# Kernel tuning notes

Measured on AMD Instinct MI355X. Metric: run time of the kernel, lower is better.

The kernel has to match this reference:

```python
import jax, jax.numpy as jnp
import numpy as np

B, T, HID = 2, 2048, 2048
H, HKV, HD = 16, 4, 128
GROUPS = H // HKV  # num_query_groups
THETA = 10000.0
SCALE = HD ** -0.5


def setup_inputs() -> dict:
    key = jax.random.key(0)
    ks = jax.random.split(key, 5)
    std = 0.02
    return {
        "x": jax.random.normal(ks[0], (B, T, HID), jnp.float32),
        "Wq": jax.random.normal(ks[1], (HID, H * HD), jnp.float32) * std,
        "Wk": jax.random.normal(ks[2], (HID, HKV * HD), jnp.float32) * std,
        "Wv": jax.random.normal(ks[3], (HID, HKV * HD), jnp.float32) * std,
        "Wo": jax.random.normal(ks[4], (H * HD, HID), jnp.float32) * std,
    }


def _rope(x):
    # x: [B, heads, T, HD]; standard LLaMA-style rotate-half RoPE
    t = x.shape[2]
    inv_freq = 1.0 / (THETA ** (jnp.arange(0, HD, 2, dtype=jnp.float32) / HD))  # [HD/2]
    ang = jnp.arange(t, dtype=jnp.float32)[:, None] * inv_freq[None, :]  # [T, HD/2]
    cos = jnp.concatenate([jnp.cos(ang), jnp.cos(ang)], axis=-1)[None, None]  # [1,1,T,HD]
    sin = jnp.concatenate([jnp.sin(ang), jnp.sin(ang)], axis=-1)[None, None]
    x1, x2 = jnp.split(x, 2, axis=-1)
    rot = jnp.concatenate([-x2, x1], axis=-1)
    return x * cos + rot * sin


def reference(x, Wq, Wk, Wv, Wo):
    b, t, _ = x.shape
    q = (x @ Wq).reshape(b, t, H, HD).transpose(0, 2, 1, 3)      # [B,H,T,HD]
    k = (x @ Wk).reshape(b, t, HKV, HD).transpose(0, 2, 1, 3)    # [B,HKV,T,HD]
    v = (x @ Wv).reshape(b, t, HKV, HD).transpose(0, 2, 1, 3)
    q = _rope(q)
    k = _rope(k)
    # GQA: repeat_interleave kv heads along head dim
    k = jnp.repeat(k, GROUPS, axis=1)  # [B,H,T,HD]
    v = jnp.repeat(v, GROUPS, axis=1)
    scores = jnp.einsum("bhqd,bhkd->bhqk", q, k) * SCALE  # [B,H,T,T]
    causal = jnp.tril(jnp.ones((t, t), dtype=bool))
    scores = jnp.where(causal[None, None], scores, jnp.finfo(scores.dtype).min)
    attn = jax.nn.softmax(scores, axis=-1)
    out = jnp.einsum("bhqk,bhkd->bhqd", attn, v)  # [B,H,T,HD]
    out = out.transpose(0, 2, 1, 3).reshape(b, t, H * HD)
    return out @ Wo
```

## Files before the change

kernel.cpp:

```cpp
#include <hip/hip_runtime.h>
#include <hip/hip_bf16.h>

#define B_   2
#define T_   2048
#define HID_ 2048
#define H_   16
#define HKV_ 4
#define HD_  128
#define NQKV 3072
#define M_   4096
#define SCALE_ 0.08838834764831845f

using f32x4 = __attribute__((ext_vector_type(4))) float;
using s16x8 = __attribute__((ext_vector_type(8))) short;
using u16x8 = __attribute__((ext_vector_type(8))) unsigned short;

typedef const __attribute__((address_space(1))) unsigned int* gptr_t;
typedef __attribute__((address_space(3))) unsigned int* lptr_t;

__device__ __forceinline__ unsigned short f2bf(float f) {
  __hip_bfloat16 h = __float2bfloat16(f);
  return *reinterpret_cast<unsigned short*>(&h);
}
__device__ __forceinline__ float bf2f(unsigned short u) {
  union { unsigned int u; float f; } x;
  x.u = ((unsigned int)u) << 16;
  return x.f;
}

__global__ void cast_bf16_k(const float* __restrict__ in, unsigned short* __restrict__ out, int n8) {
  int i = blockIdx.x * 256 + threadIdx.x;
  if (i >= n8) return;
  float4 v0 = ((const float4*)in)[i * 2];
  float4 v1 = ((const float4*)in)[i * 2 + 1];
  u16x8 o;
  o[0] = f2bf(v0.x); o[1] = f2bf(v0.y); o[2] = f2bf(v0.z); o[3] = f2bf(v0.w);
  o[4] = f2bf(v1.x); o[5] = f2bf(v1.y); o[6] = f2bf(v1.z); o[7] = f2bf(v1.w);
  ((u16x8*)out)[i] = o;
}

__global__ void transpose_cast_k(const float* __restrict__ in, unsigned short* __restrict__ out,
                                 int R, int C) {
  __shared__ float tile[32][33];
  const int tc = blockIdx.x * 32, tr = blockIdx.y * 32;
  const int lx = threadIdx.x & 31, ly = threadIdx.x >> 5;
#pragma unroll
  for (int i = 0; i < 32; i += 8) tile[ly + i][lx] = in[(long)(tr + ly + i) * C + tc + lx];
  __syncthreads();
#pragma unroll
  for (int i = 0; i < 32; i += 8)
    out[(long)(tc + ly + i) * R + tr + lx] = f2bf(tile[lx][ly + i]);
}

__global__ void transpose_v_k(const unsigned short* __restrict__ qkv, unsigned short* __restrict__ vtp) {
  __shared__ unsigned short tile[32][33];
  const int b = blockIdx.z;
  const int t0 = blockIdx.x * 32, n0 = blockIdx.y * 32;
  const int lx = threadIdx.x & 31, ly = threadIdx.x >> 5;
#pragma unroll
  for (int i = 0; i < 32; i += 8)
    tile[ly + i][lx] = qkv[(long)(b * T_ + t0 + ly + i) * NQKV + 2560 + n0 + lx];
  __syncthreads();
#pragma unroll
  for (int i = 0; i < 32; i += 8)
    vtp[(long)(b * 512 + n0 + ly + i) * T_ + t0 + lx] = tile[lx][ly + i];
}

__global__ void rope_table_k(float* __restrict__ cosT, float* __restrict__ sinT) {
  int idx = blockIdx.x * 256 + threadIdx.x;
  int tt = idx >> 6, i = idx & 63;
  float inv = powf(10000.0f, -(float)i * (1.0f / 64.0f));
  float ang = (float)tt * inv;
  cosT[idx] = cosf(ang);
  sinT[idx] = sinf(ang);
}

__global__ void rope_apply_k(unsigned short* __restrict__ qkv,
                             const float* __restrict__ cosT, const float* __restrict__ sinT) {
  int idx = blockIdx.x * 256 + threadIdx.x;
  int g = idx & 7;
  int r = idx >> 3;
  int hh = r % 20;
  int m = r / 20;
  int tt = m & (T_ - 1);
  int col = ((hh < 16) ? hh * 128 : 2048 + (hh - 16) * 128) + g * 8;
  float scl = (hh < 16) ? SCALE_ : 1.0f;
  unsigned short* p = qkv + (long)m * NQKV + col;
  u16x8 lo = *(const u16x8*)(p);
  u16x8 hi = *(const u16x8*)(p + 64);
  const float4* cp = (const float4*)(cosT + tt * 64 + g * 8);
  const float4* sp = (const float4*)(sinT + tt * 64 + g * 8);
  float c[8], s[8];
  { float4 a = cp[0], b = cp[1]; c[0]=a.x;c[1]=a.y;c[2]=a.z;c[3]=a.w;c[4]=b.x;c[5]=b.y;c[6]=b.z;c[7]=b.w; }
  { float4 a = sp[0], b = sp[1]; s[0]=a.x;s[1]=a.y;s[2]=a.z;s[3]=a.w;s[4]=b.x;s[5]=b.y;s[6]=b.z;s[7]=b.w; }
  u16x8 olo, ohi;
#pragma unroll
  for (int j = 0; j < 8; ++j) {
    float x0 = bf2f(lo[j]), x1 = bf2f(hi[j]);
    olo[j] = f2bf((x0 * c[j] - x1 * s[j]) * scl);
    ohi[j] = f2bf((x1 * c[j] + x0 * s[j]) * scl);
  }
  *(u16x8*)(p) = olo;
  *(u16x8*)(p + 64) = ohi;
}

template <bool BF16OUT>
__global__ __launch_bounds__(256) void gemm_bt(const short* __restrict__ A, const short* __restrict__ Bt,
                                               void* __restrict__ Cv, int M, int N, int K) {
  __shared__ short lA[4096];
  __shared__ short lB[4096];
  const int t = threadIdx.x;
  const int l = t & 63;
  const int w = t >> 6;
  const int wr = (w >> 1) * 64, wc = (w & 1) * 64;
  const int lr = l & 15, lk = (l >> 4) * 8;

  const short* Ag = A + (long)(blockIdx.x * 128 + (t >> 2)) * K + (t & 3) * 8;
  const short* Bg = Bt + (long)(blockIdx.y * 128 + (t >> 2)) * K + (t & 3) * 8;

  f32x4 acc[4][4] = {};

  for (int k0 = 0; k0 < K; k0 += 32) {
    __builtin_amdgcn_global_load_lds((gptr_t)(Ag + k0),                (lptr_t)&lA[t * 8],        16, 0, 0);
    __builtin_amdgcn_global_load_lds((gptr_t)(Ag + (long)64 * K + k0), (lptr_t)&lA[2048 + t * 8], 16, 0, 0);
    __builtin_amdgcn_global_load_lds((gptr_t)(Bg + k0),                (lptr_t)&lB[t * 8],        16, 0, 0);
    __builtin_amdgcn_global_load_lds((gptr_t)(Bg + (long)64 * K + k0), (lptr_t)&lB[2048 + t * 8], 16, 0, 0);
    __syncthreads();
    s16x8 af[4], bfr[4];
#pragma unroll
    for (int m = 0; m < 4; ++m) af[m] = *(const s16x8*)&lA[(wr + m * 16 + lr) * 32 + lk];
#pragma unroll
    for (int n = 0; n < 4; ++n) bfr[n] = *(const s16x8*)&lB[(wc + n * 16 + lr) * 32 + lk];
#pragma unroll
    for (int m = 0; m < 4; ++m)
#pragma unroll
      for (int n = 0; n < 4; ++n)
        acc[m][n] = __builtin_amdgcn_mfma_f32_16x16x32_bf16(af[m], bfr[n], acc[m][n], 0, 0, 0);
    __syncthreads();
  }

#pragma unroll
  for (int m = 0; m < 4; ++m) {
    const int row0 = blockIdx.x * 128 + wr + m * 16 + (l >> 4) * 4;
#pragma unroll
    for (int n = 0; n < 4; ++n) {
      const int col = blockIdx.y * 128 + wc + n * 16 + lr;
#pragma unroll
      for (int r = 0; r < 4; ++r) {
        float v = acc[m][n][r];
        if constexpr (BF16OUT)
          ((unsigned short*)Cv)[(long)(row0 + r) * N + col] = f2bf(v);
        else
          ((float*)Cv)[(long)(row0 + r) * N + col] = v;
      }
    }
  }
}

__global__ __launch_bounds__(256, 2) void attn_kernel(const short* __restrict__ qkv,
                                                      const short* __restrict__ vt,
                                                      unsigned short* __restrict__ outp) {
  const int pj = blockIdx.x;
  const int bh = blockIdx.y;
  const int b = bh >> 4, h = bh & 15, hkv = h >> 2;
  const int tid = threadIdx.x, w = tid >> 6, l = tid & 63;
  const int lr = l & 15, lg = l >> 4;

  __shared__ short lK[2][8192];
  __shared__ short lP[4][16 * 72];

  const short* kb = qkv + (long)(b * T_) * NQKV + 2048 + hkv * HD_;
  const short* vb = vt + (long)(b * 512 + hkv * HD_) * T_;
  short* pw = &lP[w][0];

  auto STAGE = [&](int buf, int kvt) {
#pragma unroll
    for (int i = 0; i < 4; ++i) {
      int flat16 = i * 256 + tid;
      int r = flat16 >> 4;
      int cb = (flat16 & 15) << 4;
      int scb = cb ^ ((r & 7) << 4);
      const short* src = kb + (long)(kvt * 64 + r) * NQKV + (scb >> 1);
      __builtin_amdgcn_global_load_lds((gptr_t)src, (lptr_t)&lK[buf][flat16 * 8], 16, 0, 0);
    }
  };

#pragma unroll 1
  for (int ph = 0; ph < 2; ++ph) {
    const int qtile = ph ? 31 - pj : pj;
    const int ntiles = qtile + 1;

    const short* qp = qkv + (long)(b * T_ + qtile * 64 + w * 16 + lr) * NQKV + h * HD_;
    s16x8 qf[4];
#pragma unroll
    for (int ks = 0; ks < 4; ++ks) qf[ks] = *(const s16x8*)(qp + ks * 32 + lg * 8);

    f32x4 o[8] = {};
    float mrun[4], lrun[4];
#pragma unroll
    for (int r = 0; r < 4; ++r) { mrun[r] = -1e30f; lrun[r] = 0.f; }

    STAGE(0, 0);
    __syncthreads();
    int cur = 0;

    for (int kvt = 0; kvt < ntiles; ++kvt) {
      if (kvt + 1 < ntiles) STAGE(cur ^ 1, kvt + 1);

      s16x8 vf[2][8];
#pragma unroll
      for (int ks2 = 0; ks2 < 2; ++ks2)
#pragma unroll
        for (int db = 0; db < 8; ++db)
          vf[ks2][db] = *(const s16x8*)(vb + (long)(db * 16 + lr) * T_ + kvt * 64 + ks2 * 32 + lg * 8);

      const char* lkb = (const char*)&lK[cur][0];
      f32x4 s[4] = {};
#pragma unroll
      for (int nb = 0; nb < 4; ++nb) {
        const int row = nb * 16 + lr;
        const int rb = row * 256;
        const int xr = (row & 7) << 4;
#pragma unroll
        for (int ks = 0; ks < 4; ++ks) {
          s16x8 kf = *(const s16x8*)(lkb + (rb + ((ks * 64 + lg * 16) ^ xr)));
          s[nb] = __builtin_amdgcn_mfma_f32_16x16x32_bf16(qf[ks], kf, s[nb], 0, 0, 0);
        }
      }
      if (kvt == qtile) {
#pragma unroll
        for (int nb = 0; nb < 4; ++nb)
#pragma unroll
          for (int r = 0; r < 4; ++r)
            if (nb * 16 + lr > w * 16 + lg * 4 + r) s[nb][r] = -1e30f;
      }
      float sc[4];
#pragma unroll
      for (int r = 0; r < 4; ++r) {
        float v = fmaxf(fmaxf(s[0][r], s[1][r]), fmaxf(s[2][r], s[3][r]));
        v = fmaxf(v, __shfl_xor(v, 1));
        v = fmaxf(v, __shfl_xor(v, 2));
        v = fmaxf(v, __shfl_xor(v, 4));
        v = fmaxf(v, __shfl_xor(v, 8));
        float mnew = fmaxf(mrun[r], v);
        sc[r] = __expf(mrun[r] - mnew);
        mrun[r] = mnew;
      }
      float ps[4] = {0.f, 0.f, 0.f, 0.f};
#pragma unroll
      for (int nb = 0; nb < 4; ++nb)
#pragma unroll
        for (int r = 0; r < 4; ++r) {
          float p = __expf(s[nb][r] - mrun[r]);
          s[nb][r] = p;
          ps[r] += p;
        }
#pragma unroll
      for (int r = 0; r < 4; ++r) {
        ps[r] += __shfl_xor(ps[r], 1);
        ps[r] += __shfl_xor(ps[r], 2);
        ps[r] += __shfl_xor(ps[r], 4);
        ps[r] += __shfl_xor(ps[r], 8);
        lrun[r] = lrun[r] * sc[r] + ps[r];
      }
#pragma unroll
      for (int db = 0; db < 8; ++db)
#pragma unroll
        for (int r = 0; r < 4; ++r) o[db][r] *= sc[r];
#pragma unroll
      for (int nb = 0; nb < 4; ++nb)
#pragma unroll
        for (int r = 0; r < 4; ++r)
          pw[(lg * 4 + r) * 72 + nb * 16 + lr] = (short)f2bf(s[nb][r]);
#pragma unroll
      for (int ks2 = 0; ks2 < 2; ++ks2) {
        s16x8 pf = *(const s16x8*)&pw[lr * 72 + ks2 * 32 + lg * 8];
#pragma unroll
        for (int db = 0; db < 8; ++db)
          o[db] = __builtin_amdgcn_mfma_f32_16x16x32_bf16(pf, vf[ks2][db], o[db], 0, 0, 0);
      }
      __syncthreads();
      cur ^= 1;
    }

    unsigned short* ob = outp + (long)(b * T_ + qtile * 64 + w * 16) * HID_ + h * HD_;
#pragma unroll
    for (int db = 0; db < 8; ++db)
#pragma unroll
      for (int r = 0; r < 4; ++r)
        ob[(long)(lg * 4 + r) * HID_ + db * 16 + lr] = f2bf(o[db][r] / lrun[r]);
  }
}

extern "C" void kernel_launch(void* const* d_in, const int* in_sizes, int n_in,
                              void* d_out, int out_size, void* d_ws, size_t ws_size,
                              hipStream_t stream) {
  (void)in_sizes; (void)n_in; (void)out_size; (void)ws_size;
  const float* x  = (const float*)d_in[0];
  const float* Wq = (const float*)d_in[1];
  const float* Wk = (const float*)d_in[2];
  const float* Wv = (const float*)d_in[3];
  const float* Wo = (const float*)d_in[4];
  float* outp = (float*)d_out;

  char* wsp = (char*)d_ws;
  auto take = [&](size_t bytes) { char* p = wsp; wsp += (bytes + 255) & ~(size_t)255; return p; };
  unsigned short* xb    = (unsigned short*)take((size_t)M_ * HID_ * 2);
  unsigned short* WqkvT = (unsigned short*)take((size_t)NQKV * HID_ * 2);
  unsigned short* WoT   = (unsigned short*)take((size_t)HID_ * HID_ * 2);
  unsigned short* QKV   = (unsigned short*)take((size_t)M_ * NQKV * 2);
  unsigned short* Vtb   = (unsigned short*)take((size_t)1024 * T_ * 2);
  unsigned short* AO    = (unsigned short*)take((size_t)M_ * HID_ * 2);
  float* cosT = (float*)take((size_t)T_ * 64 * 4);
  float* sinT = (float*)take((size_t)T_ * 64 * 4);

  cast_bf16_k<<<4096, 256, 0, stream>>>(x, xb, M_ * HID_ / 8);
  transpose_cast_k<<<dim3(64, 64), 256, 0, stream>>>(Wq, WqkvT, 2048, 2048);
  transpose_cast_k<<<dim3(16, 64), 256, 0, stream>>>(Wk, WqkvT + (size_t)2048 * 2048, 2048, 512);
  transpose_cast_k<<<dim3(16, 64), 256, 0, stream>>>(Wv, WqkvT + (size_t)2560 * 2048, 2048, 512);
  transpose_cast_k<<<dim3(64, 64), 256, 0, stream>>>(Wo, WoT, 2048, 2048);
  rope_table_k<<<512, 256, 0, stream>>>(cosT, sinT);

  gemm_bt<true><<<dim3(32, 24), 256, 0, stream>>>((const short*)xb, (const short*)WqkvT,
                                                  (void*)QKV, M_, NQKV, HID_);
  rope_apply_k<<<(M_ * 20 * 8) / 256, 256, 0, stream>>>(QKV, cosT, sinT);
  transpose_v_k<<<dim3(64, 16, 2), 256, 0, stream>>>(QKV, Vtb);

  attn_kernel<<<dim3(16, 32), 256, 0, stream>>>((const short*)QKV, (const short*)Vtb, AO);

  gemm_bt<false><<<dim3(32, 16), 256, 0, stream>>>((const short*)AO, (const short*)WoT,
                                                   (void*)outp, M_, HID_, HID_);
}
```

Baseline: 398.7 us.

## Replace GEMMs with larger-tile triple-buffered kernel and split attention query tiles

Both projection GEMMs now use a templated 512-thread kernel with 256x256 or 256x128 tiles, a three-stage LDS ring with swizzled layout, explicit vmcnt waits and MFMA priority boosting. The goal is more reuse per block and less time stalled on global loads. The attention kernel no longer pairs two query tiles per block; it launches one block per query tile, heaviest first, and raises the occupancy hint to 3. This gives finer load balancing, but some blocks become short and the large GEMM tiles leave fewer blocks to fill the CUs.

After: 568.7 us. 42.6% more time.

```diff
diff --git a/kernel.cpp b/kernel.cpp
--- a/kernel.cpp
+++ b/kernel.cpp
@@ -104,47 +104,93 @@
   *(u16x8*)(p + 64) = ohi;
 }
 
-template <bool BF16OUT>
-__global__ __launch_bounds__(256) void gemm_bt(const short* __restrict__ A, const short* __restrict__ Bt,
-                                               void* __restrict__ Cv, int M, int N, int K) {
-  __shared__ short lA[4096];
-  __shared__ short lB[4096];
-  const int t = threadIdx.x;
-  const int l = t & 63;
-  const int w = t >> 6;
-  const int wr = (w >> 1) * 64, wc = (w & 1) * 64;
-  const int lr = l & 15, lk = (l >> 4) * 8;
-
-  const short* Ag = A + (long)(blockIdx.x * 128 + (t >> 2)) * K + (t & 3) * 8;
-  const short* Bg = Bt + (long)(blockIdx.y * 128 + (t >> 2)) * K + (t & 3) * 8;
-
-  f32x4 acc[4][4] = {};
-
-  for (int k0 = 0; k0 < K; k0 += 32) {
-    __builtin_amdgcn_global_load_lds((gptr_t)(Ag + k0),                (lptr_t)&lA[t * 8],        16, 0, 0);
-    __builtin_amdgcn_global_load_lds((gptr_t)(Ag + (long)64 * K + k0), (lptr_t)&lA[2048 + t * 8], 16, 0, 0);
-    __builtin_amdgcn_global_load_lds((gptr_t)(Bg + k0),                (lptr_t)&lB[t * 8],        16, 0, 0);
-    __builtin_amdgcn_global_load_lds((gptr_t)(Bg + (long)64 * K + k0), (lptr_t)&lB[2048 + t * 8], 16, 0, 0);
-    __syncthreads();
-    s16x8 af[4], bfr[4];
-#pragma unroll
-    for (int m = 0; m < 4; ++m) af[m] = *(const s16x8*)&lA[(wr + m * 16 + lr) * 32 + lk];
-#pragma unroll
-    for (int n = 0; n < 4; ++n) bfr[n] = *(const s16x8*)&lB[(wc + n * 16 + lr) * 32 + lk];
-#pragma unroll
-    for (int m = 0; m < 4; ++m)
-#pragma unroll
-      for (int n = 0; n < 4; ++n)
-        acc[m][n] = __builtin_amdgcn_mfma_f32_16x16x32_bf16(af[m], bfr[n], acc[m][n], 0, 0, 0);
-    __syncthreads();
-  }
-
-#pragma unroll
-  for (int m = 0; m < 4; ++m) {
-    const int row0 = blockIdx.x * 128 + wr + m * 16 + (l >> 4) * 4;
-#pragma unroll
-    for (int n = 0; n < 4; ++n) {
-      const int col = blockIdx.y * 128 + wc + n * 16 + lr;
+template <int BM, int BN, int WM, int WN, bool BF16OUT>
+__global__ __launch_bounds__(512, 2) void gemm8(const short* __restrict__ A, const short* __restrict__ Bt,
+                                                void* __restrict__ Cv, int M, int N, int K) {
+  constexpr int BK = 32;
+  constexpr int MR = BM / WM / 16;
+  constexpr int NR = BN / WN / 16;
+  constexpr int TILE = (BM + BN) * BK;
+  constexpr int ACH = BM * 4;
+  constexpr int CHUNKS = (BM + BN) * 4;
+  constexpr int LPT = CHUNKS / 512;
+  __shared__ short lds[3 * TILE];
+
+  const int tid = threadIdx.x, l = tid & 63, w = tid >> 6;
+  const int wm = w % WM, wn = w / WM;
+  const int lr = l & 15, lg = l >> 4;
+
+  const short* sp[LPT];
+  int dst[LPT];
+#pragma unroll
+  for (int j = 0; j < LPT; ++j) {
+    int c = j * 512 + tid;
+    bool isA = (j * 512 < ACH);
+    int cc = isA ? c : c - ACH;
+    int row = cc >> 2;
+    int soff = ((cc & 3) << 3) ^ (((row >> 1) & 3) << 3);
+    sp[j] = (isA ? A + (long)(blockIdx.x * BM + row) * K
+                 : Bt + (long)(blockIdx.y * BN + row) * K) + soff;
+    dst[j] = c * 8;
+  }
+
+  auto STAGE = [&](int t, int buf) {
+#pragma unroll
+    for (int j = 0; j < LPT; ++j)
+      __builtin_amdgcn_global_load_lds((gptr_t)(sp[j] + t * 32), (lptr_t)&lds[buf * TILE + dst[j]], 16, 0, 0);
+  };
+
+  f32x4 acc[MR][NR] = {};
+  const int NT = K >> 5;
+
+  STAGE(0, 0);
+  STAGE(1, 1);
+  if constexpr (LPT == 4) asm volatile("s_waitcnt vmcnt(4)" ::: "memory");
+  else                    asm volatile("s_waitcnt vmcnt(3)" ::: "memory");
+  __builtin_amdgcn_s_barrier();
+  asm volatile("" ::: "memory");
+
+  for (int t = 0; t < NT; ++t) {
+    if (t + 2 < NT) STAGE(t + 2, (t + 2) % 3);
+
+    const short* bufp = &lds[(t % 3) * TILE];
+    s16x8 af[MR], bfv[NR];
+#pragma unroll
+    for (int m = 0; m < MR; ++m) {
+      const int row = wm * (MR * 16) + m * 16 + lr;
+      af[m] = *(const s16x8*)&bufp[row * 32 + ((lg * 8) ^ (((row >> 1) & 3) << 3))];
+    }
+#pragma unroll
+    for (int n = 0; n < NR; ++n) {
+      const int row = wn * (NR * 16) + n * 16 + lr;
+      bfv[n] = *(const s16x8*)&bufp[BM * 32 + row * 32 + ((lg * 8) ^ (((row >> 1) & 3) << 3))];
+    }
+    __builtin_amdgcn_s_setprio(1);
+#pragma unroll
+    for (int m = 0; m < MR; ++m)
+#pragma unroll
+      for (int n = 0; n < NR; ++n)
+        acc[m][n] = __builtin_amdgcn_mfma_f32_16x16x32_bf16(af[m], bfv[n], acc[m][n], 0, 0, 0);
+    __builtin_amdgcn_s_setprio(0);
+
+    if (t + 1 < NT) {
+      if (t + 2 < NT) {
+        if constexpr (LPT == 4) asm volatile("s_waitcnt vmcnt(4)" ::: "memory");
+        else                    asm volatile("s_waitcnt vmcnt(3)" ::: "memory");
+      } else {
+        asm volatile("s_waitcnt vmcnt(0)" ::: "memory");
+      }
+      __builtin_amdgcn_s_barrier();
+      asm volatile("" ::: "memory");
+    }
+  }
+
+#pragma unroll
+  for (int m = 0; m < MR; ++m) {
+    const int row0 = blockIdx.x * BM + wm * (MR * 16) + m * 16 + lg * 4;
+#pragma unroll
+    for (int n = 0; n < NR; ++n) {
+      const int col = blockIdx.y * BN + wn * (NR * 16) + n * 16 + lr;
 #pragma unroll
       for (int r = 0; r < 4; ++r) {
         float v = acc[m][n][r];
@@ -157,10 +203,10 @@
   }
 }
 
-__global__ __launch_bounds__(256, 2) void attn_kernel(const short* __restrict__ qkv,
+__global__ __launch_bounds__(256, 3) void attn_kernel(const short* __restrict__ qkv,
                                                       const short* __restrict__ vt,
                                                       unsigned short* __restrict__ outp) {
-  const int pj = blockIdx.x;
+  const int qtile = 31 - blockIdx.x;
   const int bh = blockIdx.y;
   const int b = bh >> 4, h = bh & 15, hkv = h >> 2;
   const int tid = threadIdx.x, w = tid >> 6, l = tid & 63;
@@ -185,111 +231,107 @@
     }
   };
 
-#pragma unroll 1
-  for (int ph = 0; ph < 2; ++ph) {
-    const int qtile = ph ? 31 - pj : pj;
-    const int ntiles = qtile + 1;
-
-    const short* qp = qkv + (long)(b * T_ + qtile * 64 + w * 16 + lr) * NQKV + h * HD_;
-    s16x8 qf[4];
-#pragma unroll
-    for (int ks = 0; ks < 4; ++ks) qf[ks] = *(const s16x8*)(qp + ks * 32 + lg * 8);
-
-    f32x4 o[8] = {};
-    float mrun[4], lrun[4];
-#pragma unroll
-    for (int r = 0; r < 4; ++r) { mrun[r] = -1e30f; lrun[r] = 0.f; }
-
-    STAGE(0, 0);
+  const int ntiles = qtile + 1;
+
+  const short* qp = qkv + (long)(b * T_ + qtile * 64 + w * 16 + lr) * NQKV + h * HD_;
+  s16x8 qf[4];
+#pragma unroll
+  for (int ks = 0; ks < 4; ++ks) qf[ks] = *(const s16x8*)(qp + ks * 32 + lg * 8);
+
+  f32x4 o[8] = {};
+  float mrun[4], lrun[4];
+#pragma unroll
+  for (int r = 0; r < 4; ++r) { mrun[r] = -1e30f; lrun[r] = 0.f; }
+
+  STAGE(0, 0);
+  __syncthreads();
+  int cur = 0;
+
+  for (int kvt = 0; kvt < ntiles; ++kvt) {
+    if (kvt + 1 < ntiles) STAGE(cur ^ 1, kvt + 1);
+
+    s16x8 vf[2][8];
+#pragma unroll
+    for (int ks2 = 0; ks2 < 2; ++ks2)
+#pragma unroll
+      for (int db = 0; db < 8; ++db)
+        vf[ks2][db] = *(const s16x8*)(vb + (long)(db * 16 + lr) * T_ + kvt * 64 + ks2 * 32 + lg * 8);
+
+    const char* lkb = (const char*)&lK[cur][0];
+    f32x4 s[4] = {};
+#pragma unroll
+    for (int nb = 0; nb < 4; ++nb) {
+      const int row = nb * 16 + lr;
+      const int rb = row * 256;
+      const int xr = (row & 7) << 4;
+#pragma unroll
+      for (int ks = 0; ks < 4; ++ks) {
+        s16x8 kf = *(const s16x8*)(lkb + (rb + ((ks * 64 + lg * 16) ^ xr)));
+        s[nb] = __builtin_amdgcn_mfma_f32_16x16x32_bf16(qf[ks], kf, s[nb], 0, 0, 0);
+      }
+    }
+    if (kvt == qtile) {
+#pragma unroll
+      for (int nb = 0; nb < 4; ++nb)
+#pragma unroll
+        for (int r = 0; r < 4; ++r)
+          if (nb * 16 + lr > w * 16 + lg * 4 + r) s[nb][r] = -1e30f;
+    }
+    float sc[4];
+#pragma unroll
+    for (int r = 0; r < 4; ++r) {
+      float v = fmaxf(fmaxf(s[0][r], s[1][r]), fmaxf(s[2][r], s[3][r]));
+      v = fmaxf(v, __shfl_xor(v, 1));
+      v = fmaxf(v, __shfl_xor(v, 2));
+      v = fmaxf(v, __shfl_xor(v, 4));
+      v = fmaxf(v, __shfl_xor(v, 8));
+      float mnew = fmaxf(mrun[r], v);
+      sc[r] = __expf(mrun[r] - mnew);
+      mrun[r] = mnew;
+    }
+    float ps[4] = {0.f, 0.f, 0.f, 0.f};
+#pragma unroll
+    for (int nb = 0; nb < 4; ++nb)
+#pragma unroll
+      for (int r = 0; r < 4; ++r) {
+        float p = __expf(s[nb][r] - mrun[r]);
+        s[nb][r] = p;
+        ps[r] += p;
+      }
+#pragma unroll
+    for (int r = 0; r < 4; ++r) {
+      ps[r] += __shfl_xor(ps[r], 1);
+      ps[r] += __shfl_xor(ps[r], 2);
+      ps[r] += __shfl_xor(ps[r], 4);
+      ps[r] += __shfl_xor(ps[r], 8);
+      lrun[r] = lrun[r] * sc[r] + ps[r];
+    }
+#pragma unroll
+    for (int db = 0; db < 8; ++db)
+#pragma unroll
+      for (int r = 0; r < 4; ++r) o[db][r] *= sc[r];
+#pragma unroll
+    for (int nb = 0; nb < 4; ++nb)
+#pragma unroll
+      for (int r = 0; r < 4; ++r)
+        pw[(lg * 4 + r) * 72 + nb * 16 + lr] = (short)f2bf(s[nb][r]);
+#pragma unroll
+    for (int ks2 = 0; ks2 < 2; ++ks2) {
+      s16x8 pf = *(const s16x8*)&pw[lr * 72 + ks2 * 32 + lg * 8];
+#pragma unroll
+      for (int db = 0; db < 8; ++db)
+        o[db] = __builtin_amdgcn_mfma_f32_16x16x32_bf16(pf, vf[ks2][db], o[db], 0, 0, 0);
+    }
     __syncthreads();
-    int cur = 0;
-
-    for (int kvt = 0; kvt < ntiles; ++kvt) {
-      if (kvt + 1 < ntiles) STAGE(cur ^ 1, kvt + 1);
-
-      s16x8 vf[2][8];
-#pragma unroll
-      for (int ks2 = 0; ks2 < 2; ++ks2)
-#pragma unroll
-        for (int db = 0; db < 8; ++db)
-          vf[ks2][db] = *(const s16x8*)(vb + (long)(db * 16 + lr) * T_ + kvt * 64 + ks2 * 32 + lg * 8);
-
-      const char* lkb = (const char*)&lK[cur][0];
-      f32x4 s[4] = {};
-#pragma unroll
-      for (int nb = 0; nb < 4; ++nb) {
-        const int row = nb * 16 + lr;
-        const int rb = row * 256;
-        const int xr = (row & 7) << 4;
-#pragma unroll
-        for (int ks = 0; ks < 4; ++ks) {
-          s16x8 kf = *(const s16x8*)(lkb + (rb + ((ks * 64 + lg * 16) ^ xr)));
-          s[nb] = __builtin_amdgcn_mfma_f32_16x16x32_bf16(qf[ks], kf, s[nb], 0, 0, 0);
-        }
-      }
-      if (kvt == qtile) {
-#pragma unroll
-        for (int nb = 0; nb < 4; ++nb)
-#pragma unroll
-          for (int r = 0; r < 4; ++r)
-            if (nb * 16 + lr > w * 16 + lg * 4 + r) s[nb][r] = -1e30f;
-      }
-      float sc[4];
-#pragma unroll
-      for (int r = 0; r < 4; ++r) {
-        float v = fmaxf(fmaxf(s[0][r], s[1][r]), fmaxf(s[2][r], s[3][r]));
-        v = fmaxf(v, __shfl_xor(v, 1));
-        v = fmaxf(v, __shfl_xor(v, 2));
-        v = fmaxf(v, __shfl_xor(v, 4));
-        v = fmaxf(v, __shfl_xor(v, 8));
-        float mnew = fmaxf(mrun[r], v);
-        sc[r] = __expf(mrun[r] - mnew);
-        mrun[r] = mnew;
-      }
-      float ps[4] = {0.f, 0.f, 0.f, 0.f};
-#pragma unroll
-      for (int nb = 0; nb < 4; ++nb)
-#pragma unroll
-        for (int r = 0; r < 4; ++r) {
-          float p = __expf(s[nb][r] - mrun[r]);
-          s[nb][r] = p;
-          ps[r] += p;
-        }
-#pragma unroll
-      for (int r = 0; r < 4; ++r) {
-        ps[r] += __shfl_xor(ps[r], 1);
-        ps[r] += __shfl_xor(ps[r], 2);
-        ps[r] += __shfl_xor(ps[r], 4);
-        ps[r] += __shfl_xor(ps[r], 8);
-        lrun[r] = lrun[r] * sc[r] + ps[r];
-      }
-#pragma unroll
-      for (int db = 0; db < 8; ++db)
-#pragma unroll
-        for (int r = 0; r < 4; ++r) o[db][r] *= sc[r];
-#pragma unroll
-      for (int nb = 0; nb < 4; ++nb)
-#pragma unroll
-        for (int r = 0; r < 4; ++r)
-          pw[(lg * 4 + r) * 72 + nb * 16 + lr] = (short)f2bf(s[nb][r]);
-#pragma unroll
-      for (int ks2 = 0; ks2 < 2; ++ks2) {
-        s16x8 pf = *(const s16x8*)&pw[lr * 72 + ks2 * 32 + lg * 8];
-#pragma unroll
-        for (int db = 0; db < 8; ++db)
-          o[db] = __builtin_amdgcn_mfma_f32_16x16x32_bf16(pf, vf[ks2][db], o[db], 0, 0, 0);
-      }
-      __syncthreads();
-      cur ^= 1;
-    }
-
-    unsigned short* ob = outp + (long)(b * T_ + qtile * 64 + w * 16) * HID_ + h * HD_;
-#pragma unroll
-    for (int db = 0; db < 8; ++db)
-#pragma unroll
-      for (int r = 0; r < 4; ++r)
-        ob[(long)(lg * 4 + r) * HID_ + db * 16 + lr] = f2bf(o[db][r] / lrun[r]);
-  }
+    cur ^= 1;
+  }
+
+  unsigned short* ob = outp + (long)(b * T_ + qtile * 64 + w * 16) * HID_ + h * HD_;
+#pragma unroll
+  for (int db = 0; db < 8; ++db)
+#pragma unroll
+    for (int r = 0; r < 4; ++r)
+      ob[(long)(lg * 4 + r) * HID_ + db * 16 + lr] = f2bf(o[db][r] / lrun[r]);
 }
 
 extern "C" void kernel_launch(void* const* d_in, const int* in_sizes, int n_in,
@@ -321,13 +363,13 @@
   transpose_cast_k<<<dim3(64, 64), 256, 0, stream>>>(Wo, WoT, 2048, 2048);
   rope_table_k<<<512, 256, 0, stream>>>(cosT, sinT);
 
-  gemm_bt<true><<<dim3(32, 24), 256, 0, stream>>>((const short*)xb, (const short*)WqkvT,
-                                                  (void*)QKV, M_, NQKV, HID_);
+  gemm8<256, 256, 2, 4, true><<<dim3(16, 12), 512, 0, stream>>>((const short*)xb, (const short*)WqkvT,
+                                                                (void*)QKV, M_, NQKV, HID_);
   rope_apply_k<<<(M_ * 20 * 8) / 256, 256, 0, stream>>>(QKV, cosT, sinT);
   transpose_v_k<<<dim3(64, 16, 2), 256, 0, stream>>>(QKV, Vtb);
 
-  attn_kernel<<<dim3(16, 32), 256, 0, stream>>>((const short*)QKV, (const short*)Vtb, AO);
-
-  gemm_bt<false><<<dim3(32, 16), 256, 0, stream>>>((const short*)AO, (const short*)WoT,
-                                                   (void*)outp, M_, HID_, HID_);
-}
+  attn_kernel<<<dim3(32, 32), 256, 0, stream>>>((const short*)QKV, (const short*)Vtb, AO);
+
+  gemm8<256, 128, 4, 2, false><<<dim3(16, 16), 512, 0, stream>>>((const short*)AO, (const short*)WoT,
+                                                                 (void*)outp, M_, HID_, HID_);
+}
```
